# Performance work log

Hardware: AMD Instinct MI355X
Metric: run time of the kernel (lower is better)

## Reference

```python
import jax, jax.numpy as jnp
import numpy as np

V = 64          # len(tokens)
HID = 512       # hidden_size
N = 2048        # n rollouts
MAX_LEN = 64
MIN_LEN = 4


def setup_inputs() -> dict:
    key = jax.random.key(0)
    k = jax.random.split(key, 6)
    return {
        "input_init": jax.random.uniform(k[0], (1, 2 * V), dtype=jnp.float32),
        "hidden_init": jax.random.uniform(k[1], (1, HID), dtype=jnp.float32),
        "Wx": jax.random.normal(k[2], (2 * V, HID), dtype=jnp.float32) * 0.05,
        "Wh": jax.random.normal(k[3], (HID, HID), dtype=jnp.float32) * 0.05,
        "b": jnp.zeros((HID,), jnp.float32),
        "Wp": jax.random.normal(k[4], (HID, V), dtype=jnp.float32) * 0.05,
        "bp": jnp.zeros((V,), jnp.float32),
        "two_arity": jnp.arange(0, 6, dtype=jnp.int32),    # binary operators
        "one_arity": jnp.arange(6, 14, dtype=jnp.int32),   # unary operators
        "var_tokens": jnp.arange(14, 22, dtype=jnp.int32), # variable terminals
        "n": N,
    }


def _forward(input_init, hidden_init, Wx, Wh, b, Wp, bp, two_arity, one_arity, var_tokens, n):
    ids = jnp.arange(V)
    two_vec = (ids[:, None] == two_arity[None, :]).any(-1)
    one_vec = (ids[:, None] == one_arity[None, :]).any(-1)
    zero_vec = ~(two_vec | one_vec)
    var_vec = (ids[:, None] == var_tokens[None, :]).any(-1)
    const_vec = zero_vec & ~var_vec

    def isin(tok, arr):
        return (tok[:, None] == arr[None, :]).any(-1)

    def upd_arity(tok, c):  # update_arity from the source
        return c - 1 + 2 * isin(tok, two_arity).astype(jnp.int32) + isin(tok, one_arity).astype(jnp.int32)

    def parent_sibling(seq, t):  # _get_parent_sibling: backward scan over tokens 0..t
        nn, L = seq.shape
        def body(k, st):
            ps, c = st
            i = t - k
            valid = i >= 0
            ic = jnp.maximum(i, 0)
            tok = seq[:, ic]
            c = jnp.where(valid, upd_arity(tok, c), c)
            cmask = valid & (c == 0) & jnp.all(ps == -1, axis=1)
            sib = jnp.where(i == t, -1, seq[:, jnp.minimum(ic + 1, L - 1)])
            cand = jnp.stack([tok, sib], axis=1)
            return (jnp.where(cmask[:, None], cand, ps), c)
        ps, _ = jax.lax.fori_loop(0, L, body,
                                  (-jnp.ones((nn, 2), jnp.int32), jnp.zeros((nn,), jnp.int32)))
        recent = seq[:, t]
        rec_is_op = ~zero_vec[recent]  # most recent token is an operator -> it is the parent
        rec_ps = jnp.stack([recent, -jnp.ones_like(recent)], axis=1)
        return jnp.where(rec_is_op[:, None], rec_ps, ps)

    x0 = jnp.tile(input_init, (n, 1))
    h0 = jnp.tile(hidden_init, (n, 1))  # NOTE: original loop never updates hidden state
    skey = jax.random.key(1234)

    def step(carry, t):
        x, counters, alive, seq = carry
        h = jnp.tanh(x @ Wx + h0 @ Wh + b)      # SimpleRNN cell step (tanh)
        probs = jax.nn.softmax(h @ Wp + bp)     # Dense projection + softmax
        tot = t + counters                      # current length + open slots
        keep = jnp.ones((n, V), bool)
        keep = keep & ~(zero_vec[None, :] & (tot < MIN_LEN)[:, None])          # MinLengthConstraint
        keep = keep & ~(two_vec[None, :] & (tot + 2 > MAX_LEN)[:, None])       # MaxLengthConstraint
        keep = keep & ~(one_vec[None, :] & (tot + 1 > MAX_LEN)[:, None])
        has_var = (seq[:, :, None] == var_tokens[None, None, :]).any((1, 2))   # MinVariableExpression
        keep = keep & ~(const_vec[None, :] & ((~has_var) & (counters == 1))[:, None])
        probs = jnp.where(keep, probs, 0.0)
        probs = probs / jnp.maximum(probs.sum(-1, keepdims=True), 1e-30)       # normalize
        logp_safe = jnp.log(jnp.where(probs > 0, probs, 1.0))
        logits = jnp.where(probs > 0, logp_safe, -jnp.inf)
        tokens = jax.random.categorical(jax.random.fold_in(skey, t), logits).astype(jnp.int32)
        lp = jnp.take_along_axis(logp_safe, tokens[:, None], axis=1)[:, 0]
        ent = jnp.sum(jnp.where(probs > 0, -probs * logp_safe, 0.0), axis=1)
        counters = upd_arity(tokens, counters)
        alive = alive & (counters > 0)
        seq = seq.at[:, t].set(tokens)
        ps = parent_sibling(seq, t)
        x_next = jnp.concatenate([jax.nn.one_hot(ps[:, 0], V, dtype=x.dtype),
                                  jax.nn.one_hot(ps[:, 1], V, dtype=x.dtype)], axis=1)
        return (x_next, counters, alive, seq), (alive, ent, lp)

    init = (x0, jnp.ones((n,), jnp.int32), jnp.ones((n,), bool), -jnp.ones((n, MAX_LEN), jnp.int32))
    (_, _, _, seq), (mask, ents, lps) = jax.lax.scan(step, init, jnp.arange(MAX_LEN))
    mask = mask.T                              # [n, L]
    m = mask.astype(ents.dtype)
    lengths = mask.sum(-1).astype(jnp.int32) + 1
    return seq, lengths, (ents.T * m).sum(-1), (lps.T * m).sum(-1)


def reference(input_init, hidden_init, Wx, Wh, b, Wp, bp, two_arity, one_arity, var_tokens, n):
    return _forward(input_init, hidden_init, Wx, Wh, b, Wp, bp, two_arity, one_arity, var_tokens, n)
```

## Files before the change

kernel.cpp:

```cpp
#include <hip/hip_runtime.h>
#include <stdint.h>
#include <math.h>

#define NSEQ   2048
#define VV     64
#define HID    512
#define LMAX   64
#define MINLEN 4
#define H_ROWS 4226
#define H_T0   4225

__device__ __forceinline__ uint32_t rotl32(uint32_t x, int r) {
  return (x << r) | (x >> (32 - r));
}
__device__ __forceinline__ void threefry2x32(uint32_t ks0, uint32_t ks1,
                                             uint32_t x0, uint32_t x1,
                                             uint32_t &o0, uint32_t &o1) {
  uint32_t ks2 = ks0 ^ ks1 ^ 0x1BD11BDAu;
  x0 += ks0; x1 += ks1;
#define TF_RND(r) { x0 += x1; x1 = rotl32(x1, (r)); x1 ^= x0; }
  TF_RND(13) TF_RND(15) TF_RND(26) TF_RND(6)
  x0 += ks1; x1 += ks2 + 1u;
  TF_RND(17) TF_RND(29) TF_RND(16) TF_RND(24)
  x0 += ks2; x1 += ks0 + 2u;
  TF_RND(13) TF_RND(15) TF_RND(26) TF_RND(6)
  x0 += ks0; x1 += ks1 + 3u;
  TF_RND(17) TF_RND(29) TF_RND(16) TF_RND(24)
  x0 += ks1; x1 += ks2 + 4u;
  TF_RND(13) TF_RND(15) TF_RND(26) TF_RND(6)
  x0 += ks2; x1 += ks0 + 5u;
#undef TF_RND
  o0 = x0; o1 = x1;
}

__device__ __forceinline__ float wgum(uint32_t k0, uint32_t k1, uint32_t idx) {
  uint32_t b0, b1;
  threefry2x32(k0, k1, 0u, idx, b0, b1);
  const uint32_t bits = b0 ^ b1;
  const float f = __uint_as_float((bits >> 9) | 0x3f800000u) - 1.0f;
  const float u = (f == 0.f) ? 1.17549435e-38f : f;
  return -logf(u);
}

template <int CTRL>
__device__ __forceinline__ float dppf(float v) {
  return __int_as_float(__builtin_amdgcn_update_dpp(
      __float_as_int(v), __float_as_int(v), CTRL, 0xF, 0xF, false));
}
__device__ __forceinline__ float wave_max_bcast(float v) {
  v = fmaxf(v, dppf<0x121>(v));
  v = fmaxf(v, dppf<0x122>(v));
  v = fmaxf(v, dppf<0x124>(v));
  v = fmaxf(v, dppf<0x128>(v));
  v = fmaxf(v, dppf<0x142>(v));
  v = fmaxf(v, dppf<0x143>(v));
  return __int_as_float(__builtin_amdgcn_readlane(__float_as_int(v), 63));
}
__device__ __forceinline__ float wave_sum_bcast(float v) {
  v += dppf<0x121>(v);
  v += dppf<0x122>(v);
  v += dppf<0x124>(v);
  v += dppf<0x128>(v);
  v += dppf<0x142>(v);
  v += dppf<0x143>(v);
  return __int_as_float(__builtin_amdgcn_readlane(__float_as_int(v), 63));
}

__global__ void rnn_precompute(const float *__restrict__ input_init,
                               const float *__restrict__ hidden_init,
                               const float *__restrict__ Wx,
                               const float *__restrict__ Wh,
                               const float *__restrict__ b,
                               float *__restrict__ hconst,
                               float *__restrict__ xw0,
                               uint32_t *__restrict__ ktab) {
  const int k = blockIdx.x * 64 + threadIdx.x;
  if (blockIdx.x == 0) {
    const int t = threadIdx.x;
    uint32_t o0, o1;
    threefry2x32(0u, 1234u, 0u, (uint32_t)t, o0, o1);
    ktab[2 * t]     = o0;
    ktab[2 * t + 1] = o1;
  }
  if (k >= HID) return;
  double acc = 0.0;
  for (int j = 0; j < HID; ++j)
    acc = fma((double)hidden_init[j], (double)Wh[(size_t)j * HID + k], acc);
  hconst[k] = (float)(acc + (double)b[k]);
  double a2 = 0.0;
  for (int j = 0; j < 2 * VV; ++j)
    a2 = fma((double)input_init[j], (double)Wx[(size_t)j * HID + k], a2);
  xw0[k] = (float)a2;
}

__global__ __launch_bounds__(512) void rnn_xtable(
    const float *__restrict__ Wx, const float *__restrict__ Wp,
    const float *__restrict__ bp,
    const float *__restrict__ hconst, const float *__restrict__ xw0,
    const int *__restrict__ two_arr, int n2,
    const int *__restrict__ one_arr, int n1,
    float *__restrict__ X) {
  __shared__ float  smh[HID];
  __shared__ double smpart[8][VV];

  const int r   = blockIdx.x;
  const int tid = threadIdx.x;

  if (r != H_T0) {
    const int p = r / 65 - 1;
    if (p >= 0) {
      bool isOp = false;
      for (int j = 0; j < n2; ++j) isOp |= (p == two_arr[j]);
      for (int j = 0; j < n1; ++j) isOp |= (p == one_arr[j]);
      if (!isOp) return;
    }
  }

  {
    float ax;
    if (r == H_T0) {
      ax = xw0[tid];
    } else {
      const int p = r / 65 - 1;
      const int s = r % 65 - 1;
      ax = 0.f;
      if (p >= 0) ax = Wx[(size_t)p * HID + tid];
      if (s >= 0) ax += Wx[(size_t)(VV + s) * HID + tid];
    }
    smh[tid] = tanhf(ax + hconst[tid]);
  }
  __syncthreads();

  const int v  = tid & 63;
  const int sl = tid >> 6;
  double acc = 0.0;
  for (int k = sl * 64; k < sl * 64 + 64; ++k)
    acc = fma((double)smh[k], (double)Wp[(size_t)k * VV + v], acc);
  smpart[sl][v] = acc;
  __syncthreads();

  if (tid < VV) {
    double s = 0.0;
#pragma unroll
    for (int i = 0; i < 8; ++i) s += smpart[i][tid];
    X[(size_t)r * VV + tid] = (float)(s + (double)bp[tid]);
  }
}

__global__ __launch_bounds__(64) void rnn_sampler(
    const float *__restrict__ Wx, const float *__restrict__ Wp,
    const float *__restrict__ bp,
    const float *__restrict__ hconst_g, const float *__restrict__ xw0_g,
    const int *__restrict__ two_arr, int n2,
    const int *__restrict__ one_arr, int n1,
    const int *__restrict__ var_arr, int nv,
    const float *__restrict__ Xtab, const uint32_t *__restrict__ ktab,
    int useX,
    float *__restrict__ out) {
  const int lane = threadIdx.x;
  const int n    = blockIdx.x;
  const uint32_t idx = (uint32_t)((n << 6) + lane);

  bool isTwo = false, isOne = false, isVar = false;
  for (int j = 0; j < n2; ++j) isTwo |= (lane == two_arr[j]);
  for (int j = 0; j < n1; ++j) isOne |= (lane == one_arr[j]);
  for (int j = 0; j < nv; ++j) isVar |= (lane == var_arr[j]);
  const unsigned long long two_mask = __ballot(isTwo);
  const unsigned long long one_mask = __ballot(isOne);
  const unsigned long long var_mask = __ballot(isVar);
  const bool two_v   = (two_mask >> lane) & 1ull;
  const bool one_v   = (one_mask >> lane) & 1ull;
  const bool zero_v  = !(two_v || one_v);
  const bool const_v = zero_v && !((var_mask >> lane) & 1ull);
  const float bp_v   = bp[lane];

  float hc[8], xw[8];
  if (!useX) {
#pragma unroll
    for (int i = 0; i < 8; ++i) {
      hc[i] = hconst_g[i * 64 + lane];
      xw[i] = xw0_g[i * 64 + lane];
    }
  }

  int myseq = -1;
  unsigned long long twoHist = 0ull, oneHist = 0ull;
  int counters = 1;
  bool alive = true, hasvar = false;
  float accE = 0.f, accLP = 0.f;
  int lenacc = 0;
  int row = H_T0;

  float w = wgum(ktab[0], ktab[1], idx);

  for (int t = 0; t < LMAX; ++t) {
    float w_nxt = 1.f;
    if (t + 1 < LMAX)
      w_nxt = wgum(ktab[2 * (t + 1)], ktab[2 * (t + 1) + 1], idx);

    float x;
    if (useX) {
      x = Xtab[(size_t)row * VV + lane];
    } else {
      float hreg[8];
#pragma unroll
      for (int i = 0; i < 8; ++i) {
        float ax;
        if (row == H_T0) {
          ax = xw[i];
        } else {
          const int p  = row / 65 - 1;
          const int sb = row % 65 - 1;
          ax = 0.f;
          if (p >= 0) ax = Wx[(size_t)p * HID + i * 64 + lane];
          if (sb >= 0) ax += Wx[(size_t)(VV + sb) * HID + i * 64 + lane];
        }
        hreg[i] = (float)tanh((double)(ax + hc[i]));
      }
      float acc = 0.f;
#pragma unroll
      for (int i = 0; i < 8; ++i) {
        for (int j = 0; j < 64; ++j) {
          const float hk = __int_as_float(
              __builtin_amdgcn_readlane(__float_as_int(hreg[i]), j));
          acc = fmaf(hk, Wp[(size_t)(i * 64 + j) * VV + lane], acc);
        }
      }
      x = acc + bp_v;
    }

    const int tot = t + counters;
    bool keep = true;
    if (zero_v && tot < MINLEN) keep = false;
    if (two_v && (tot + 2 > LMAX)) keep = false;
    if (one_v && (tot + 1 > LMAX)) keep = false;
    if (const_v && !hasvar && (counters == 1)) keep = false;

    const float ex  = expf(x);
    const float val = keep ? (ex / w) : 0.f;
    const float mv  = wave_max_bcast(val);
    const unsigned long long win = __ballot(val == mv);
    const int token = __ffsll((long long)win) - 1;

    const bool tk2 = (two_mask >> token) & 1ull;
    const bool tk1 = (one_mask >> token) & 1ull;
    const bool tkv = (var_mask >> token) & 1ull;

    if (lane == t) myseq = token;
    twoHist = (twoHist << 1) | (unsigned long long)(tk2 ? 1 : 0);
    oneHist = (oneHist << 1) | (unsigned long long)(tk1 ? 1 : 0);

    counters += -1 + 2 * (int)tk2 + (int)tk1;
    const bool aliveN = alive && (counters > 0);

    if (alive) {
      const float ek = keep ? ex : 0.f;
      const float s2 = wave_sum_bcast(ek);
      const float dd = wave_sum_bcast(ek * x);
      const float logS2 = logf(s2);
      const int tok_u = __builtin_amdgcn_readfirstlane(token);
      const float x_tok = __int_as_float(
          __builtin_amdgcn_readlane(__float_as_int(x), tok_u));
      if (aliveN) {
        accLP += x_tok - logS2;
        accE  += logS2 - dd / s2;
        lenacc++;
      }
    }
    alive = aliveN;
    hasvar = hasvar || tkv;

    int parent, sib;
    if (tk2 || tk1) {
      parent = token; sib = -1;
    } else {
      const unsigned long long mle = (2ull << lane) - 1ull;
      const int c = 2 * __popcll(twoHist & mle) + __popcll(oneHist & mle) -
                    (lane + 1);
      const unsigned long long hb = __ballot((lane <= t) && (c == 0));
      if (hb == 0ull) {
        parent = -1; sib = -1;
      } else {
        int kf = __ffsll((long long)hb) - 1;
        kf = __builtin_amdgcn_readfirstlane(kf);
        parent = __builtin_amdgcn_readlane(myseq, t - kf);
        sib = (kf == 0) ? -1 : __builtin_amdgcn_readlane(myseq, t - kf + 1);
      }
    }
    row = (parent + 1) * 65 + (sib + 1);
    w = w_nxt;
  }

  out[(size_t)n * LMAX + lane] = (float)myseq;
  if (lane == 0) {
    out[(size_t)NSEQ * LMAX + n]       = (float)(lenacc + 1);
    out[(size_t)NSEQ * (LMAX + 1) + n] = accE;
    out[(size_t)NSEQ * (LMAX + 2) + n] = accLP;
  }
}

extern "C" void kernel_launch(void *const *d_in, const int *in_sizes, int n_in,
                              void *d_out, int out_size, void *d_ws, size_t ws_size,
                              hipStream_t stream) {
  (void)n_in; (void)out_size;
  const float *input_init  = (const float *)d_in[0];
  const float *hidden_init = (const float *)d_in[1];
  const float *Wx = (const float *)d_in[2];
  const float *Wh = (const float *)d_in[3];
  const float *b  = (const float *)d_in[4];
  const float *Wp = (const float *)d_in[5];
  const float *bp = (const float *)d_in[6];
  const int *two_arr = (const int *)d_in[7];
  const int *one_arr = (const int *)d_in[8];
  const int *var_arr = (const int *)d_in[9];
  const int n2 = in_sizes[7], n1 = in_sizes[8], nv = in_sizes[9];

  const size_t offK = 4096;
  const size_t offX = 8192;
  const size_t szX  = (size_t)H_ROWS * VV * sizeof(float);
  const int useX = (ws_size >= offX + szX) ? 1 : 0;

  float    *hconst = (float *)d_ws;
  float    *xw0    = hconst + HID;
  uint32_t *ktab   = (uint32_t *)((char *)d_ws + offK);
  float    *Xtab   = (float *)((char *)d_ws + offX);
  float    *out    = (float *)d_out;

  rnn_precompute<<<8, 64, 0, stream>>>(input_init, hidden_init, Wx, Wh, b,
                                       hconst, xw0, ktab);
  if (useX)
    rnn_xtable<<<H_ROWS, 512, 0, stream>>>(Wx, Wp, bp, hconst, xw0,
                                           two_arr, n2, one_arr, n1, Xtab);

  rnn_sampler<<<NSEQ, 64, 0, stream>>>(Wx, Wp, bp, hconst, xw0,
                                       two_arr, n2, one_arr, n1,
                                       var_arr, nv, Xtab, ktab, useX, out);
}
```

Before: 102.8 us.

## Precompute Gumbel noise table in a parallel kernel and sample in log space

Moves threefry random generation and the Gumbel transform out of the serial per-step sampler loop into a separate fully parallel kernel that writes a 32 MB noise table, which the sampler then reads each step. Sampling switches from exp(x)/w to the additive Gumbel-max form g + x, and expf is only evaluated for alive sequences. The cost is an extra launch plus about 32 MB of global writes and reads. The extra log and the changed comparison could alter tie-breaking relative to the previous ratio form.

After: 124.0 us. 20.6% more time.

```diff
diff --git a/kernel.cpp b/kernel.cpp
--- a/kernel.cpp
+++ b/kernel.cpp
@@ -33,13 +33,14 @@
   o0 = x0; o1 = x1;
 }
 
-__device__ __forceinline__ float wgum(uint32_t k0, uint32_t k1, uint32_t idx) {
+__device__ __forceinline__ float gumbel_bits(uint32_t k0, uint32_t k1,
+                                             uint32_t idx) {
   uint32_t b0, b1;
   threefry2x32(k0, k1, 0u, idx, b0, b1);
   const uint32_t bits = b0 ^ b1;
   const float f = __uint_as_float((bits >> 9) | 0x3f800000u) - 1.0f;
   const float u = (f == 0.f) ? 1.17549435e-38f : f;
-  return -logf(u);
+  return -logf(-logf(u));
 }
 
 template <int CTRL>
@@ -147,6 +148,14 @@
   }
 }
 
+__global__ __launch_bounds__(256) void rnn_gumbel_table(
+    const uint32_t *__restrict__ ktab, float *__restrict__ g) {
+  const int t   = blockIdx.y;
+  const int idx = blockIdx.x * 256 + threadIdx.x;
+  g[(size_t)t * (NSEQ * VV) + idx] =
+      gumbel_bits(ktab[2 * t], ktab[2 * t + 1], (uint32_t)idx);
+}
+
 __global__ __launch_bounds__(64) void rnn_sampler(
     const float *__restrict__ Wx, const float *__restrict__ Wp,
     const float *__restrict__ bp,
@@ -154,8 +163,8 @@
     const int *__restrict__ two_arr, int n2,
     const int *__restrict__ one_arr, int n1,
     const int *__restrict__ var_arr, int nv,
-    const float *__restrict__ Xtab, const uint32_t *__restrict__ ktab,
-    int useX,
+    const float *__restrict__ Xtab, const float *__restrict__ gtab,
+    const uint32_t *__restrict__ ktab, int useX, int useG,
     float *__restrict__ out) {
   const int lane = threadIdx.x;
   const int n    = blockIdx.x;
@@ -191,12 +200,13 @@
   int lenacc = 0;
   int row = H_T0;
 
-  float w = wgum(ktab[0], ktab[1], idx);
+  float g32 = useG ? gtab[idx] : gumbel_bits(ktab[0], ktab[1], idx);
 
   for (int t = 0; t < LMAX; ++t) {
-    float w_nxt = 1.f;
+    float g_nxt = 0.f;
     if (t + 1 < LMAX)
-      w_nxt = wgum(ktab[2 * (t + 1)], ktab[2 * (t + 1) + 1], idx);
+      g_nxt = useG ? gtab[(size_t)(t + 1) * (NSEQ * VV) + idx]
+                   : gumbel_bits(ktab[2 * (t + 1)], ktab[2 * (t + 1) + 1], idx);
 
     float x;
     if (useX) {
@@ -236,8 +246,7 @@
     if (one_v && (tot + 1 > LMAX)) keep = false;
     if (const_v && !hasvar && (counters == 1)) keep = false;
 
-    const float ex  = expf(x);
-    const float val = keep ? (ex / w) : 0.f;
+    const float val = keep ? (g32 + x) : -__builtin_inff();
     const float mv  = wave_max_bcast(val);
     const unsigned long long win = __ballot(val == mv);
     const int token = __ffsll((long long)win) - 1;
@@ -254,6 +263,7 @@
     const bool aliveN = alive && (counters > 0);
 
     if (alive) {
+      const float ex = expf(x);
       const float ek = keep ? ex : 0.f;
       const float s2 = wave_sum_bcast(ek);
       const float dd = wave_sum_bcast(ek * x);
@@ -288,7 +298,7 @@
       }
     }
     row = (parent + 1) * 65 + (sib + 1);
-    w = w_nxt;
+    g32 = g_nxt;
   }
 
   out[(size_t)n * LMAX + lane] = (float)myseq;
@@ -318,21 +328,29 @@
   const size_t offK = 4096;
   const size_t offX = 8192;
   const size_t szX  = (size_t)H_ROWS * VV * sizeof(float);
+  const size_t offG = (offX + szX + 255) & ~(size_t)255;
+  const size_t szG  = (size_t)LMAX * NSEQ * VV * sizeof(float);
   const int useX = (ws_size >= offX + szX) ? 1 : 0;
+  const int useG = (ws_size >= offG + szG) ? 1 : 0;
 
   float    *hconst = (float *)d_ws;
   float    *xw0    = hconst + HID;
   uint32_t *ktab   = (uint32_t *)((char *)d_ws + offK);
   float    *Xtab   = (float *)((char *)d_ws + offX);
+  float    *gtab   = (float *)((char *)d_ws + offG);
   float    *out    = (float *)d_out;
 
   rnn_precompute<<<8, 64, 0, stream>>>(input_init, hidden_init, Wx, Wh, b,
                                        hconst, xw0, ktab);
+  if (useG)
+    rnn_gumbel_table<<<dim3((NSEQ * VV) / 256, LMAX), 256, 0, stream>>>(ktab,
+                                                                        gtab);
   if (useX)
     rnn_xtable<<<H_ROWS, 512, 0, stream>>>(Wx, Wp, bp, hconst, xw0,
                                            two_arr, n2, one_arr, n1, Xtab);
 
   rnn_sampler<<<NSEQ, 64, 0, stream>>>(Wx, Wp, bp, hconst, xw0,
                                        two_arr, n2, one_arr, n1,
-                                       var_arr, nv, Xtab, ktab, useX, out);
-}
+                                       var_arr, nv, Xtab, gtab, ktab,
+                                       useX, useG, out);
+}
```
